# Kernel tuning notes

Measured on AMD Instinct MI355X. Metric: run time of the kernel, lower is better.

## Reference

```python
import jax, jax.numpy as jnp
import numpy as np


def _bilerp(img, x, y):
    # img: (B, C, H, W); x, y: (B, Q) pixel coords. Clamped-border bilinear sampling.
    H, W = img.shape[-2], img.shape[-1]
    x = jnp.clip(x, 0.0, W - 1.0)
    y = jnp.clip(y, 0.0, H - 1.0)
    x0 = jnp.floor(x)
    y0 = jnp.floor(y)
    x1 = jnp.minimum(x0 + 1.0, W - 1.0)
    y1 = jnp.minimum(y0 + 1.0, H - 1.0)
    wx = (x - x0)[:, None, :]
    wy = (y - y0)[:, None, :]
    x0i = x0.astype(jnp.int32); x1i = x1.astype(jnp.int32)
    y0i = y0.astype(jnp.int32); y1i = y1.astype(jnp.int32)
    gather = jax.vmap(lambda im, yi, xi: im[:, yi, xi])  # per-batch fancy gather -> (C, Q)
    v00 = gather(img, y0i, x0i)
    v01 = gather(img, y0i, x1i)
    v10 = gather(img, y1i, x0i)
    v11 = gather(img, y1i, x1i)
    top = v00 * (1.0 - wx) + v01 * wx
    bot = v10 * (1.0 - wx) + v11 * wx
    return top * (1.0 - wy) + bot * wy  # (B, C, Q)


def _forward(f0, f1, f2, grid, adjust_w, adjust_b, offset_w, offset_b, weight, bias):
    feats = [f0, f1, f2]
    B, P, S, _ = grid.shape
    C = adjust_w.shape[0]  # adjusted_channels
    # 1x1 channel-adjust conv on every level
    fa = [jnp.einsum('oc,bchw->bohw', adjust_w, f) + adjust_b[None, :, None, None] for f in feats]
    # 1x1 offset-prediction conv on the high-res level -> (B, 2S, H0, W0)
    offsets = jnp.einsum('oc,bchw->bohw', offset_w, fa[0]) + offset_b[None, :, None, None]
    gx = grid[..., 0].reshape(B, -1)  # (B, P*S), normalized [-1, 1]
    gy = grid[..., 1].reshape(B, -1)
    H0, W0 = offsets.shape[-2], offsets.shape[-1]
    # sample the predicted offsets at each grid point (align_corners=True mapping)
    ox = (gx + 1.0) * 0.5 * (W0 - 1)
    oy = (gy + 1.0) * 0.5 * (H0 - 1)
    off = _bilerp(offsets, ox, oy)  # (B, 2S, P*S)
    off5 = off.reshape(B, S, 2, P, S)
    idx = jnp.arange(S)
    sel = off5[:, idx, :, :, idx]  # (S, B, 2, P): sample point s uses offset pair s
    off_ps = jnp.transpose(sel, (1, 3, 0, 2))  # (B, P, S, 2) = (dy, dx) in pixels
    dy = off_ps[..., 0].reshape(B, -1)
    dx = off_ps[..., 1].reshape(B, -1)
    outs = []
    for f in fa:
        Hl, Wl = f.shape[-2], f.shape[-1]
        px = (gx + 1.0) * 0.5 * (Wl - 1) + dx
        py = (gy + 1.0) * 0.5 * (Hl - 1) + dy
        s = _bilerp(f, px, py).reshape(B, C, P, S)
        s = jnp.transpose(s, (0, 2, 3, 1))  # (B, P, S, C)
        # 1x1 deform-conv weight = dense C x C mix + bias
        outs.append(jnp.einsum('bpsc,oc->bpso', s, weight) + bias)
    return jnp.stack(outs, axis=1)  # (B, n_levels, P, S, C)


def setup_inputs() -> dict:
    key = jax.random.key(0)
    k = jax.random.split(key, 10)
    B, P, S, Cin, C = 16, 768, 36, 64, 72
    shapes = [(80, 200), (40, 100), (20, 50)]
    f0 = jax.random.normal(k[0], (B, Cin, shapes[0][0], shapes[0][1]), jnp.float32)
    f1 = jax.random.normal(k[1], (B, Cin, shapes[1][0], shapes[1][1]), jnp.float32)
    f2 = jax.random.normal(k[2], (B, Cin, shapes[2][0], shapes[2][1]), jnp.float32)
    grid = jax.random.uniform(k[3], (B, P, S, 2), jnp.float32, -1.0, 1.0)
    adjust_w = jax.random.normal(k[4], (C, Cin), jnp.float32) / np.float32(np.sqrt(Cin))
    adjust_b = jax.random.normal(k[5], (C,), jnp.float32) * 0.01
    offset_w = jax.random.normal(k[6], (2 * S, C), jnp.float32) * 0.01
    offset_b = jax.random.normal(k[7], (2 * S,), jnp.float32) * 0.01
    weight = jax.random.normal(k[8], (C, C), jnp.float32) / np.float32(np.sqrt(C))
    bias = jax.random.normal(k[9], (C,), jnp.float32) * 0.01
    return {'f0': f0, 'f1': f1, 'f2': f2, 'grid': grid, 'adjust_w': adjust_w,
            'adjust_b': adjust_b, 'offset_w': offset_w, 'offset_b': offset_b,
            'weight': weight, 'bias': bias}


def reference(f0, f1, f2, grid, adjust_w, adjust_b, offset_w, offset_b, weight, bias):
    return _forward(f0, f1, f2, grid, adjust_w, adjust_b, offset_w, offset_b, weight, bias)
```

## Files before the change

kernel.cpp:

```cpp
#include <hip/hip_runtime.h>
#include <hip/hip_bf16.h>
#include <cstdint>
#include <cstddef>

#define BB   16
#define PP   768
#define SS   36
#define CIN  64
#define CC   72
#define NPTS (BB*PP*SS)
#define H0 80
#define W0 200
#define H1 40
#define W1 100
#define H2 20
#define W2_ 50

typedef float v4f    __attribute__((ext_vector_type(4)));
typedef short short8 __attribute__((ext_vector_type(8)));

static __device__ __forceinline__ unsigned short f2bf(float x) {
    unsigned u = __float_as_uint(x);
    u += 0x7fffu + ((u >> 16) & 1u);
    return (unsigned short)(u >> 16);
}
static __device__ __forceinline__ float bf2f(unsigned u16) {
    return __uint_as_float(u16 << 16);
}
static __device__ __forceinline__ void ld_pair(const unsigned short* p, float& a, float& b) {
    unsigned u = *(const unsigned*)p;
    a = __uint_as_float((u & 0xffffu) << 16);
    b = __uint_as_float((u >> 16) << 16);
}

__global__ void prep_mats(const float* __restrict__ adjust_w, const float* __restrict__ adjust_b,
                          const float* __restrict__ offset_w, const float* __restrict__ offset_b,
                          const float* __restrict__ weight,   const float* __restrict__ bias,
                          unsigned short* __restrict__ Wab, float* __restrict__ bias144) {
    int idx = blockIdx.x * 256 + threadIdx.x;
    if (idx < 4608) {
        int o = idx >> 6, k = idx & 63;
        float acc = 0.f;
        for (int c = 0; c < CC; ++c) acc += weight[o*CC + c] * adjust_w[c*CIN + k];
        Wab[o*64 + k] = f2bf(acc);
    } else if (idx < 9216) {
        int j = idx - 4608; int o = j >> 6, k = j & 63;
        float acc = 0.f;
        for (int c = 0; c < CC; ++c) acc += offset_w[o*CC + c] * adjust_w[c*CIN + k];
        Wab[(72 + o)*64 + k] = f2bf(acc);
    } else if (idx < 9288) {
        int o = idx - 9216;
        float acc = bias[o];
        for (int c = 0; c < CC; ++c) acc += weight[o*CC + c] * adjust_b[c];
        bias144[o] = acc;
    } else if (idx < 9360) {
        int o = idx - 9288;
        float acc = offset_b[o];
        for (int c = 0; c < CC; ++c) acc += offset_w[o*CC + c] * adjust_b[c];
        bias144[72 + o] = acc;
    }
}

template<int HW, int MTILES, bool WITH_OFF>
__global__ __launch_bounds__(256) void fields_mfma(
        const float* __restrict__ f,
        const unsigned short* __restrict__ Wab, const float* __restrict__ bias144,
        unsigned short* __restrict__ g_dst, unsigned short* __restrict__ off_dst) {
    __shared__ char lds[64 * 128];

    const int t = threadIdx.x;
    {
        const int pxl = t & 63;
        const int q   = t >> 6;
        const int pxg = blockIdx.x * 64 + pxl;
        const int b   = pxg / HW;
        const int rem = pxg - b * HW;
        const float* fb = f + (size_t)b * 64 * HW + rem;
        const unsigned swz = (pxl & 7) << 4;
        #pragma unroll
        for (int j = 0; j < 4; ++j) {
            const int k = j * 16 + q * 4;
            float v0 = fb[(size_t)(k + 0) * HW];
            float v1 = fb[(size_t)(k + 1) * HW];
            float v2 = fb[(size_t)(k + 2) * HW];
            float v3 = fb[(size_t)(k + 3) * HW];
            ushort4 pk;
            pk.x = f2bf(v0); pk.y = f2bf(v1); pk.z = f2bf(v2); pk.w = f2bf(v3);
            *(ushort4*)(lds + pxl * 128 + ((unsigned)(j * 32 + q * 8) ^ swz)) = pk;
        }
    }
    __syncthreads();

    const int ln  = t & 63;
    const int pxw = ((t >> 6) << 4) + (ln & 15);
    const int kg  = ln >> 4;
    const unsigned swzr = (pxw & 7) << 4;
    const short8 bf0 = *(const short8*)(lds + pxw * 128 + ((unsigned)(kg * 16)      ^ swzr));
    const short8 bf1 = *(const short8*)(lds + pxw * 128 + ((unsigned)(64 + kg * 16) ^ swzr));

    const int arow = ln & 15;
    const size_t gbase = ((size_t)blockIdx.x * 64 + pxw) * (size_t)CC;

    #pragma unroll
    for (int mt = 0; mt < MTILES; ++mt) {
        const int ch0 = mt * 16 + (kg << 2);
        v4f acc = *(const v4f*)(bias144 + ch0);
        const short8 a0 = *(const short8*)(Wab + (mt * 16 + arow) * 64 + kg * 8);
        const short8 a1 = *(const short8*)(Wab + (mt * 16 + arow) * 64 + 32 + kg * 8);
        acc = __builtin_amdgcn_mfma_f32_16x16x32_bf16(a0, bf0, acc, 0, 0, 0);
        acc = __builtin_amdgcn_mfma_f32_16x16x32_bf16(a1, bf1, acc, 0, 0, 0);
        ushort4 pk;
        pk.x = f2bf(acc[0]); pk.y = f2bf(acc[1]); pk.z = f2bf(acc[2]); pk.w = f2bf(acc[3]);
        if (ch0 < 72) {
            *(ushort4*)(g_dst + gbase + ch0) = pk;
        } else if (WITH_OFF) {
            *(ushort4*)(off_dst + gbase + (ch0 - 72)) = pk;
        }
    }
}

__global__ __launch_bounds__(256) void dydx_kernel(const float* __restrict__ grid,
                                                   const unsigned short* __restrict__ off_field,
                                                   float* __restrict__ dydx) {
    unsigned bid = blockIdx.x;
    bid = (bid & 7u) * (1728u / 8u) + (bid >> 3);
    int idx = (int)(bid * 256 + threadIdx.x);
    int s = idx % SS;
    int b = idx / (PP * SS);
    float gx = grid[2 * idx], gy = grid[2 * idx + 1];
    float ox = (gx + 1.f) * 0.5f * (W0 - 1);
    float oy = (gy + 1.f) * 0.5f * (H0 - 1);
    ox = fminf(fmaxf(ox, 0.f), (float)(W0 - 1));
    oy = fminf(fmaxf(oy, 0.f), (float)(H0 - 1));
    float x0f = floorf(ox), y0f = floorf(oy);
    float wx = ox - x0f, wy = oy - y0f;
    int x0 = (int)x0f, y0 = (int)y0f;
    int x1 = min(x0 + 1, W0 - 1), y1 = min(y0 + 1, H0 - 1);
    size_t base = (size_t)b * H0 * W0;
    int ch = 2 * s;
    float a00, b00, a01, b01, a10, b10, a11, b11;
    ld_pair(off_field + (base + (size_t)y0 * W0 + x0) * CC + ch, a00, b00);
    ld_pair(off_field + (base + (size_t)y0 * W0 + x1) * CC + ch, a01, b01);
    ld_pair(off_field + (base + (size_t)y1 * W0 + x0) * CC + ch, a10, b10);
    ld_pair(off_field + (base + (size_t)y1 * W0 + x1) * CC + ch, a11, b11);
    float top_a = a00 * (1.f - wx) + a01 * wx, bot_a = a10 * (1.f - wx) + a11 * wx;
    float top_b = b00 * (1.f - wx) + b01 * wx, bot_b = b10 * (1.f - wx) + b11 * wx;
    dydx[2 * idx]     = top_a * (1.f - wy) + bot_a * wy;
    dydx[2 * idx + 1] = top_b * (1.f - wy) + bot_b * wy;
}

__global__ __launch_bounds__(256) void sample_kernel(
        const float* __restrict__ grid, const float* __restrict__ dydx,
        const unsigned short* __restrict__ g0, const unsigned short* __restrict__ g1,
        const unsigned short* __restrict__ g2, float* __restrict__ out) {
    unsigned bid = blockIdx.x;
    bid = (bid & 7u) * (46656u / 8u) + (bid >> 3);
    size_t tid = (size_t)bid * 256 + threadIdx.x;
    int cg = (int)(tid % 9); int c0 = cg * 8;
    size_t q = tid / 9;
    int s  = (int)(q % SS);  size_t q2 = q / SS;
    int p  = (int)(q2 % PP); size_t q3 = q2 / PP;
    int l  = (int)(q3 % 3);  int b = (int)(q3 / 3);
    int pid = (b * PP + p) * SS + s;

    float gx = grid[2 * pid], gy = grid[2 * pid + 1];
    float dyv = dydx[2 * pid], dxv = dydx[2 * pid + 1];

    int Hl, Wl; const unsigned short* g;
    if (l == 0)      { Hl = H0; Wl = W0;  g = g0; }
    else if (l == 1) { Hl = H1; Wl = W1;  g = g1; }
    else             { Hl = H2; Wl = W2_; g = g2; }

    float px = (gx + 1.f) * 0.5f * (Wl - 1) + dxv;
    float py = (gy + 1.f) * 0.5f * (Hl - 1) + dyv;
    px = fminf(fmaxf(px, 0.f), (float)(Wl - 1));
    py = fminf(fmaxf(py, 0.f), (float)(Hl - 1));
    float x0f = floorf(px), y0f = floorf(py);
    float wx = px - x0f, wy = py - y0f;
    int x0 = (int)x0f, y0 = (int)y0f;
    int x1 = min(x0 + 1, Wl - 1), y1 = min(y0 + 1, Hl - 1);

    size_t base = (size_t)b * Hl * Wl;
    const unsigned short* p00 = g + (base + (size_t)y0 * Wl + x0) * CC + c0;
    const unsigned short* p01 = g + (base + (size_t)y0 * Wl + x1) * CC + c0;
    const unsigned short* p10 = g + (base + (size_t)y1 * Wl + x0) * CC + c0;
    const unsigned short* p11 = g + (base + (size_t)y1 * Wl + x1) * CC + c0;
    uint4 u00 = *(const uint4*)p00;
    uint4 u01 = *(const uint4*)p01;
    uint4 u10 = *(const uint4*)p10;
    uint4 u11 = *(const uint4*)p11;

    float w00 = (1.f - wx) * (1.f - wy), w01 = wx * (1.f - wy);
    float w10 = (1.f - wx) * wy,         w11 = wx * wy;

    const unsigned* a = (const unsigned*)&u00;
    const unsigned* bw = (const unsigned*)&u01;
    const unsigned* cw = (const unsigned*)&u10;
    const unsigned* dw = (const unsigned*)&u11;
    float o[8];
    #pragma unroll
    for (int j = 0; j < 4; ++j) {
        float a0 = bf2f(a[j] & 0xffffu),  a1 = bf2f(a[j] >> 16);
        float b0 = bf2f(bw[j] & 0xffffu), b1 = bf2f(bw[j] >> 16);
        float c0v = bf2f(cw[j] & 0xffffu), c1v = bf2f(cw[j] >> 16);
        float d0 = bf2f(dw[j] & 0xffffu), d1 = bf2f(dw[j] >> 16);
        o[2 * j]     = w00 * a0 + w01 * b0 + w10 * c0v + w11 * d0;
        o[2 * j + 1] = w00 * a1 + w01 * b1 + w10 * c1v + w11 * d1;
    }
    size_t ob = q * (size_t)CC + c0;
    v4f r0 = {o[0], o[1], o[2], o[3]};
    v4f r1 = {o[4], o[5], o[6], o[7]};
    __builtin_nontemporal_store(r0, (v4f*)&out[ob]);
    __builtin_nontemporal_store(r1, (v4f*)&out[ob + 4]);
}

extern "C" void kernel_launch(void* const* d_in, const int* in_sizes, int n_in,
                              void* d_out, int out_size, void* d_ws, size_t ws_size,
                              hipStream_t stream) {
    const float* f0       = (const float*)d_in[0];
    const float* f1       = (const float*)d_in[1];
    const float* f2       = (const float*)d_in[2];
    const float* grid     = (const float*)d_in[3];
    const float* adjust_w = (const float*)d_in[4];
    const float* adjust_b = (const float*)d_in[5];
    const float* offset_w = (const float*)d_in[6];
    const float* offset_b = (const float*)d_in[7];
    const float* weight   = (const float*)d_in[8];
    const float* bias     = (const float*)d_in[9];

    char* ws = (char*)d_ws;
    unsigned short* Wab   = (unsigned short*)(ws + 0);
    float*          b144  = (float*)(ws + 18432);
    float*          dydx  = (float*)(ws + 19200);
    unsigned short* g0    = (unsigned short*)(ws + 3558400);
    unsigned short* g1    = (unsigned short*)(ws + 40422400);
    unsigned short* g2    = (unsigned short*)(ws + 49638400);
    unsigned short* offf = (unsigned short*)d_out;

    prep_mats<<<37, 256, 0, stream>>>(adjust_w, adjust_b, offset_w, offset_b,
                                      weight, bias, Wab, b144);

    fields_mfma<16000, 9, true ><<<4000, 256, 0, stream>>>(f0, Wab, b144, g0, offf);
    fields_mfma< 4000, 5, false><<<1000, 256, 0, stream>>>(f1, Wab, b144, g1, nullptr);
    fields_mfma< 1000, 5, false><<< 250, 256, 0, stream>>>(f2, Wab, b144, g2, nullptr);

    dydx_kernel<<<1728, 256, 0, stream>>>(grid, offf, dydx);

    sample_kernel<<<46656, 256, 0, stream>>>(grid, dydx, g0, g1, g2, (float*)d_out);
}
```

Before: 166.8 us.

## Merge per-level field kernels, pack grid+offsets, process two samples per thread

Fuses the three per-level 1x1-conv MFMA kernels into one launch that dispatches on block index. The dydx kernel now writes a packed float4 of (gx, gy, dy, dx), so the sampler reads one vector load per point instead of separate grid and offset loads. The sampler processes two work items per thread with half as many blocks, cutting launch overhead and grid traffic. The cost is larger workspace use and more registers per thread in the sampler.

```diff
diff --git a/kernel.cpp b/kernel.cpp
--- a/kernel.cpp
+++ b/kernel.cpp
@@ -62,17 +62,16 @@
 }
 
 template<int HW, int MTILES, bool WITH_OFF>
-__global__ __launch_bounds__(256) void fields_mfma(
-        const float* __restrict__ f,
+static __device__ __forceinline__ void fields_body(
+        unsigned bid, const float* __restrict__ f,
         const unsigned short* __restrict__ Wab, const float* __restrict__ bias144,
-        unsigned short* __restrict__ g_dst, unsigned short* __restrict__ off_dst) {
-    __shared__ char lds[64 * 128];
-
+        unsigned short* __restrict__ g_dst, unsigned short* __restrict__ off_dst,
+        char* lds) {
     const int t = threadIdx.x;
     {
         const int pxl = t & 63;
         const int q   = t >> 6;
-        const int pxg = blockIdx.x * 64 + pxl;
+        const int pxg = (int)bid * 64 + pxl;
         const int b   = pxg / HW;
         const int rem = pxg - b * HW;
         const float* fb = f + (size_t)b * 64 * HW + rem;
@@ -99,7 +98,7 @@
     const short8 bf1 = *(const short8*)(lds + pxw * 128 + ((unsigned)(64 + kg * 16) ^ swzr));
 
     const int arow = ln & 15;
-    const size_t gbase = ((size_t)blockIdx.x * 64 + pxw) * (size_t)CC;
+    const size_t gbase = ((size_t)bid * 64 + pxw) * (size_t)CC;
 
     #pragma unroll
     for (int mt = 0; mt < MTILES; ++mt) {
@@ -119,9 +118,25 @@
     }
 }
 
+__global__ __launch_bounds__(256) void fields_all(
+        const float* __restrict__ f0, const float* __restrict__ f1, const float* __restrict__ f2,
+        const unsigned short* __restrict__ Wab, const float* __restrict__ bias144,
+        unsigned short* __restrict__ g0, unsigned short* __restrict__ g1,
+        unsigned short* __restrict__ g2, unsigned short* __restrict__ offf) {
+    __shared__ char lds[64 * 128];
+    const unsigned bid = blockIdx.x;
+    if (bid < 4000u) {
+        fields_body<16000, 9, true >(bid,         f0, Wab, bias144, g0, offf, lds);
+    } else if (bid < 5000u) {
+        fields_body< 4000, 5, false>(bid - 4000u, f1, Wab, bias144, g1, nullptr, lds);
+    } else {
+        fields_body< 1000, 5, false>(bid - 5000u, f2, Wab, bias144, g2, nullptr, lds);
+    }
+}
+
 __global__ __launch_bounds__(256) void dydx_kernel(const float* __restrict__ grid,
                                                    const unsigned short* __restrict__ off_field,
-                                                   float* __restrict__ dydx) {
+                                                   v4f* __restrict__ pdata) {
     unsigned bid = blockIdx.x;
     bid = (bid & 7u) * (1728u / 8u) + (bid >> 3);
     int idx = (int)(bid * 256 + threadIdx.x);
@@ -145,73 +160,80 @@
     ld_pair(off_field + (base + (size_t)y1 * W0 + x1) * CC + ch, a11, b11);
     float top_a = a00 * (1.f - wx) + a01 * wx, bot_a = a10 * (1.f - wx) + a11 * wx;
     float top_b = b00 * (1.f - wx) + b01 * wx, bot_b = b10 * (1.f - wx) + b11 * wx;
-    dydx[2 * idx]     = top_a * (1.f - wy) + bot_a * wy;
-    dydx[2 * idx + 1] = top_b * (1.f - wy) + bot_b * wy;
+    v4f pd;
+    pd.x = gx;
+    pd.y = gy;
+    pd.z = top_a * (1.f - wy) + bot_a * wy;
+    pd.w = top_b * (1.f - wy) + bot_b * wy;
+    pdata[idx] = pd;
 }
 
 __global__ __launch_bounds__(256) void sample_kernel(
-        const float* __restrict__ grid, const float* __restrict__ dydx,
+        const v4f* __restrict__ pdata,
         const unsigned short* __restrict__ g0, const unsigned short* __restrict__ g1,
         const unsigned short* __restrict__ g2, float* __restrict__ out) {
     unsigned bid = blockIdx.x;
-    bid = (bid & 7u) * (46656u / 8u) + (bid >> 3);
-    size_t tid = (size_t)bid * 256 + threadIdx.x;
-    int cg = (int)(tid % 9); int c0 = cg * 8;
-    size_t q = tid / 9;
-    int s  = (int)(q % SS);  size_t q2 = q / SS;
-    int p  = (int)(q2 % PP); size_t q3 = q2 / PP;
-    int l  = (int)(q3 % 3);  int b = (int)(q3 / 3);
-    int pid = (b * PP + p) * SS + s;
-
-    float gx = grid[2 * pid], gy = grid[2 * pid + 1];
-    float dyv = dydx[2 * pid], dxv = dydx[2 * pid + 1];
-
-    int Hl, Wl; const unsigned short* g;
-    if (l == 0)      { Hl = H0; Wl = W0;  g = g0; }
-    else if (l == 1) { Hl = H1; Wl = W1;  g = g1; }
-    else             { Hl = H2; Wl = W2_; g = g2; }
-
-    float px = (gx + 1.f) * 0.5f * (Wl - 1) + dxv;
-    float py = (gy + 1.f) * 0.5f * (Hl - 1) + dyv;
-    px = fminf(fmaxf(px, 0.f), (float)(Wl - 1));
-    py = fminf(fmaxf(py, 0.f), (float)(Hl - 1));
-    float x0f = floorf(px), y0f = floorf(py);
-    float wx = px - x0f, wy = py - y0f;
-    int x0 = (int)x0f, y0 = (int)y0f;
-    int x1 = min(x0 + 1, Wl - 1), y1 = min(y0 + 1, Hl - 1);
-
-    size_t base = (size_t)b * Hl * Wl;
-    const unsigned short* p00 = g + (base + (size_t)y0 * Wl + x0) * CC + c0;
-    const unsigned short* p01 = g + (base + (size_t)y0 * Wl + x1) * CC + c0;
-    const unsigned short* p10 = g + (base + (size_t)y1 * Wl + x0) * CC + c0;
-    const unsigned short* p11 = g + (base + (size_t)y1 * Wl + x1) * CC + c0;
-    uint4 u00 = *(const uint4*)p00;
-    uint4 u01 = *(const uint4*)p01;
-    uint4 u10 = *(const uint4*)p10;
-    uint4 u11 = *(const uint4*)p11;
-
-    float w00 = (1.f - wx) * (1.f - wy), w01 = wx * (1.f - wy);
-    float w10 = (1.f - wx) * wy,         w11 = wx * wy;
-
-    const unsigned* a = (const unsigned*)&u00;
-    const unsigned* bw = (const unsigned*)&u01;
-    const unsigned* cw = (const unsigned*)&u10;
-    const unsigned* dw = (const unsigned*)&u11;
-    float o[8];
+    bid = (bid & 7u) * (23328u / 8u) + (bid >> 3);
+    const size_t tbase = (size_t)bid * 512 + threadIdx.x;
     #pragma unroll
-    for (int j = 0; j < 4; ++j) {
-        float a0 = bf2f(a[j] & 0xffffu),  a1 = bf2f(a[j] >> 16);
-        float b0 = bf2f(bw[j] & 0xffffu), b1 = bf2f(bw[j] >> 16);
-        float c0v = bf2f(cw[j] & 0xffffu), c1v = bf2f(cw[j] >> 16);
-        float d0 = bf2f(dw[j] & 0xffffu), d1 = bf2f(dw[j] >> 16);
-        o[2 * j]     = w00 * a0 + w01 * b0 + w10 * c0v + w11 * d0;
-        o[2 * j + 1] = w00 * a1 + w01 * b1 + w10 * c1v + w11 * d1;
-    }
-    size_t ob = q * (size_t)CC + c0;
-    v4f r0 = {o[0], o[1], o[2], o[3]};
-    v4f r1 = {o[4], o[5], o[6], o[7]};
-    __builtin_nontemporal_store(r0, (v4f*)&out[ob]);
-    __builtin_nontemporal_store(r1, (v4f*)&out[ob + 4]);
+    for (int half = 0; half < 2; ++half) {
+        size_t tid = tbase + (size_t)half * 256;
+        int cg = (int)(tid % 9); int c0 = cg * 8;
+        size_t q = tid / 9;
+        int s  = (int)(q % SS);  size_t q2 = q / SS;
+        int p  = (int)(q2 % PP); size_t q3 = q2 / PP;
+        int l  = (int)(q3 % 3);  int b = (int)(q3 / 3);
+        int pid = (b * PP + p) * SS + s;
+
+        v4f pd = pdata[pid];
+
+        int Hl, Wl; const unsigned short* g;
+        if (l == 0)      { Hl = H0; Wl = W0;  g = g0; }
+        else if (l == 1) { Hl = H1; Wl = W1;  g = g1; }
+        else             { Hl = H2; Wl = W2_; g = g2; }
+
+        float px = (pd.x + 1.f) * 0.5f * (Wl - 1) + pd.w;
+        float py = (pd.y + 1.f) * 0.5f * (Hl - 1) + pd.z;
+        px = fminf(fmaxf(px, 0.f), (float)(Wl - 1));
+        py = fminf(fmaxf(py, 0.f), (float)(Hl - 1));
+        float x0f = floorf(px), y0f = floorf(py);
+        float wx = px - x0f, wy = py - y0f;
+        int x0 = (int)x0f, y0 = (int)y0f;
+        int x1 = min(x0 + 1, Wl - 1), y1 = min(y0 + 1, Hl - 1);
+
+        size_t base = (size_t)b * Hl * Wl;
+        const unsigned short* p00 = g + (base + (size_t)y0 * Wl + x0) * CC + c0;
+        const unsigned short* p01 = g + (base + (size_t)y0 * Wl + x1) * CC + c0;
+        const unsigned short* p10 = g + (base + (size_t)y1 * Wl + x0) * CC + c0;
+        const unsigned short* p11 = g + (base + (size_t)y1 * Wl + x1) * CC + c0;
+        uint4 u00 = *(const uint4*)p00;
+        uint4 u01 = *(const uint4*)p01;
+        uint4 u10 = *(const uint4*)p10;
+        uint4 u11 = *(const uint4*)p11;
+
+        float w00 = (1.f - wx) * (1.f - wy), w01 = wx * (1.f - wy);
+        float w10 = (1.f - wx) * wy,         w11 = wx * wy;
+
+        const unsigned* a  = (const unsigned*)&u00;
+        const unsigned* bw = (const unsigned*)&u01;
+        const unsigned* cw = (const unsigned*)&u10;
+        const unsigned* dw = (const unsigned*)&u11;
+        float o[8];
+        #pragma unroll
+        for (int j = 0; j < 4; ++j) {
+            float a0  = bf2f(a[j] & 0xffffu),  a1  = bf2f(a[j] >> 16);
+            float b0  = bf2f(bw[j] & 0xffffu), b1  = bf2f(bw[j] >> 16);
+            float c0v = bf2f(cw[j] & 0xffffu), c1v = bf2f(cw[j] >> 16);
+            float d0  = bf2f(dw[j] & 0xffffu), d1  = bf2f(dw[j] >> 16);
+            o[2 * j]     = w00 * a0 + w01 * b0 + w10 * c0v + w11 * d0;
+            o[2 * j + 1] = w00 * a1 + w01 * b1 + w10 * c1v + w11 * d1;
+        }
+        size_t ob = q * (size_t)CC + c0;
+        v4f r0 = {o[0], o[1], o[2], o[3]};
+        v4f r1 = {o[4], o[5], o[6], o[7]};
+        __builtin_nontemporal_store(r0, (v4f*)&out[ob]);
+        __builtin_nontemporal_store(r1, (v4f*)&out[ob + 4]);
+    }
 }
 
 extern "C" void kernel_launch(void* const* d_in, const int* in_sizes, int n_in,
@@ -231,20 +253,18 @@
     char* ws = (char*)d_ws;
     unsigned short* Wab   = (unsigned short*)(ws + 0);
     float*          b144  = (float*)(ws + 18432);
-    float*          dydx  = (float*)(ws + 19200);
-    unsigned short* g0    = (unsigned short*)(ws + 3558400);
-    unsigned short* g1    = (unsigned short*)(ws + 40422400);
-    unsigned short* g2    = (unsigned short*)(ws + 49638400);
+    v4f*            pdata = (v4f*)(ws + 19200);
+    unsigned short* g0    = (unsigned short*)(ws + 7097088);
+    unsigned short* g1    = (unsigned short*)(ws + 43961088);
+    unsigned short* g2    = (unsigned short*)(ws + 53177088);
     unsigned short* offf = (unsigned short*)d_out;
 
     prep_mats<<<37, 256, 0, stream>>>(adjust_w, adjust_b, offset_w, offset_b,
                                       weight, bias, Wab, b144);
 
-    fields_mfma<16000, 9, true ><<<4000, 256, 0, stream>>>(f0, Wab, b144, g0, offf);
-    fields_mfma< 4000, 5, false><<<1000, 256, 0, stream>>>(f1, Wab, b144, g1, nullptr);
-    fields_mfma< 1000, 5, false><<< 250, 256, 0, stream>>>(f2, Wab, b144, g2, nullptr);
-
-    dydx_kernel<<<1728, 256, 0, stream>>>(grid, offf, dydx);
-
-    sample_kernel<<<46656, 256, 0, stream>>>(grid, dydx, g0, g1, g2, (float*)d_out);
-}
+    fields_all<<<5250, 256, 0, stream>>>(f0, f1, f2, Wab, b144, g0, g1, g2, offf);
+
+    dydx_kernel<<<1728, 256, 0, stream>>>(grid, offf, pdata);
+
+    sample_kernel<<<23328, 256, 0, stream>>>(pdata, g0, g1, g2, (float*)d_out);
+}
```

Measured after the change: 165.1 us. About the same (-1.0%).
